# Kernel tuning notes

Hardware: AMD Instinct MI355X
Metric: run time of the kernel (lower is better)

Reference implementation:

```python
import jax, jax.numpy as jnp
import numpy as np
from jax import lax

THRESHOLDS = (0.25, 0.5, 0.75)
TAU = 100.0
NUM_CLASSES = 10
K = 32
RES_Z = 5.0
# each of the 16 binary logic gates is bilinear: g(a,b) = c0 + c1*a + c2*b + c3*a*b
GATE_COEF = jnp.array([
    [0, 0, 0, 0],   # 0: False
    [0, 0, 0, 1],   # 1: a AND b
    [0, 1, 0, -1],  # 2: a AND NOT b
    [0, 1, 0, 0],   # 3: a  (residual gate)
    [0, 0, 1, -1],  # 4: NOT a AND b
    [0, 0, 1, 0],   # 5: b
    [0, 1, 1, -2],  # 6: XOR
    [0, 1, 1, -1],  # 7: OR
    [1, -1, -1, 1], # 8: NOR
    [1, -1, -1, 2], # 9: XNOR
    [1, 0, -1, 0],  # 10: NOT b
    [1, 0, -1, 1],  # 11: a OR NOT b
    [1, -1, 0, 0],  # 12: NOT a
    [1, -1, 0, 1],  # 13: NOT a OR b
    [1, 0, 0, -1],  # 14: NAND
    [1, 0, 0, 0],   # 15: True
], dtype=jnp.float32)


def _gate_logits(key, shape):
    # residual init: pass-through gate (id 3) dominates
    w = 0.01 * jax.random.normal(key, shape, dtype=jnp.float32)
    return w.at[..., 3].add(RES_Z)


def _leaf_idx(rng, C, O, leaves=8, cpt=2, kk=9):
    # each tree uses cpt random input channels; each leaf picks one of them and a 3x3 position
    ch2 = rng.integers(0, C, size=(O, cpt))
    sel = rng.integers(0, cpt, size=(O, leaves))
    ch = np.take_along_axis(ch2, sel, axis=1)
    pos = rng.integers(0, kk, size=(O, leaves))
    return jnp.asarray(ch * kk + pos, dtype=jnp.int32)


def setup_inputs() -> dict:
    key = jax.random.key(0)
    ks = jax.random.split(key, 9)
    rng = np.random.default_rng(0)
    B = 128
    d = {"x": jax.random.uniform(ks[0], (B, 3, 32, 32), dtype=jnp.float32)}
    in_chs = [3 * len(THRESHOLDS), K, 4 * K, 16 * K]
    out_chs = [K, 4 * K, 16 * K, 32 * K]
    for i, (ci, co) in enumerate(zip(in_chs, out_chs)):
        d[f"c{i+1}_idx"] = _leaf_idx(rng, ci, co)
        d[f"c{i+1}_w"] = _gate_logits(ks[1 + i], (co, 7, 16))
    dims = [32 * K * 4, 1280 * K, 640 * K, 320 * K]
    for i in range(3):
        di, do = dims[i], dims[i + 1]
        d[f"l{i+1}_a"] = jnp.asarray(rng.integers(0, di, size=(do,)), dtype=jnp.int32)
        d[f"l{i+1}_b"] = jnp.asarray(rng.integers(0, di, size=(do,)), dtype=jnp.int32)
        d[f"l{i+1}_w"] = _gate_logits(ks[5 + i], (do, 16))
    return d


def _mix(logits):
    # softmax over 16 gates folded into 4 bilinear coefficients (fused gate mixture)
    return jax.nn.softmax(logits, axis=-1) @ GATE_COEF


def binarize(x):
    return jnp.concatenate([(x > t).astype(x.dtype) for t in THRESHOLDS], axis=1)


def tree_conv(x, leaf_idx, logits):
    # x: (B,C,H,W); leaf_idx: (O,8) into C*9 channel-major patch; logits: (O,7,16)
    B, C, H, W = x.shape
    xp = jnp.pad(x, ((0, 0), (0, 0), (1, 1), (1, 1)))
    patches = jnp.stack([xp[:, :, i:i + H, j:j + W] for i in range(3) for j in range(3)], axis=2)
    patches = patches.reshape(B, C * 9, H, W)
    vals = patches[:, leaf_idx]  # (B,O,8,H,W)
    m = _mix(logits)             # (O,7,4)
    node = 0
    for lvl in (4, 2, 1):
        a, b = vals[:, :, 0::2], vals[:, :, 1::2]
        w = m[:, node:node + lvl]  # (O,lvl,4)
        w0 = w[..., 0][None, :, :, None, None]
        w1 = w[..., 1][None, :, :, None, None]
        w2 = w[..., 2][None, :, :, None, None]
        w3 = w[..., 3][None, :, :, None, None]
        vals = w0 + w1 * a + w2 * b + w3 * (a * b)
        node += lvl
    return vals[:, :, 0]  # (B,O,H,W)


def or_pool(x):
    # OR of relaxed binary values == max pool 2x2/2
    return lax.reduce_window(x, -jnp.inf, lax.max, (1, 1, 2, 2), (1, 1, 2, 2), "VALID")


def logic_layer(x, a_idx, b_idx, logits):
    a = x[:, a_idx]  # (B,O)
    b = x[:, b_idx]
    w = _mix(logits)  # (O,4)
    return w[:, 0] + w[:, 1] * a + w[:, 2] * b + w[:, 3] * (a * b)


def group_sum(x):
    B = x.shape[0]
    return x.reshape(B, NUM_CLASSES, -1).sum(axis=-1) / TAU


def reference(x, c1_idx, c1_w, c2_idx, c2_w, c3_idx, c3_w, c4_idx, c4_w,
              l1_a, l1_b, l1_w, l2_a, l2_b, l2_w, l3_a, l3_b, l3_w):
    h = binarize(x)
    h = or_pool(tree_conv(h, c1_idx, c1_w))
    h = or_pool(tree_conv(h, c2_idx, c2_w))
    h = or_pool(tree_conv(h, c3_idx, c3_w))
    h = or_pool(tree_conv(h, c4_idx, c4_w))
    h = h.reshape(h.shape[0], -1)  # (B, 4096)
    h = logic_layer(h, l1_a, l1_b, l1_w)
    h = logic_layer(h, l2_a, l2_b, l2_w)
    h = logic_layer(h, l3_a, l3_b, l3_w)
    return group_sum(h)  # (B, 10)
```

## Files before the change

### kernel.cpp

```cpp
#include <hip/hip_runtime.h>

#define BATCH 128

typedef float v2f __attribute__((ext_vector_type(2)));
typedef float v4f __attribute__((ext_vector_type(4)));

__device__ __constant__ float GC[16][4] = {
  {0,0,0,0},{0,0,0,1},{0,1,0,-1},{0,1,0,0},
  {0,0,1,-1},{0,0,1,0},{0,1,1,-2},{0,1,1,-1},
  {1,-1,-1,1},{1,-1,-1,2},{1,0,-1,0},{1,0,-1,1},
  {1,-1,0,0},{1,-1,0,1},{1,0,0,-1},{1,0,0,0}};

__device__ __forceinline__ v2f pk_mul(v2f a, v2f b) {
  v2f d;
  asm("v_pk_mul_f32 %0, %1, %2" : "=v"(d) : "v"(a), "v"(b));
  return d;
}
__device__ __forceinline__ v2f max2(v2f a, v2f b) {
  v2f d;
  d.x = fmaxf(a.x, b.x);
  d.y = fmaxf(a.y, b.y);
  return d;
}
__device__ __forceinline__ v2f gate2pk(v2f a, v2f b, v2f w01, v2f w23) {
  v2f t = pk_mul(a, b);
  v2f d;
  asm("v_pk_fma_f32 %0, %1, %2, %2 op_sel:[0,1,0] op_sel_hi:[1,1,0]"
      : "=v"(d) : "v"(a), "v"(w01));
  asm("v_pk_fma_f32 %0, %1, %2, %0 op_sel:[0,0,0] op_sel_hi:[1,0,1]"
      : "+v"(d) : "v"(b), "v"(w23));
  asm("v_pk_fma_f32 %0, %1, %2, %0 op_sel:[0,1,0] op_sel_hi:[1,1,1]"
      : "+v"(d) : "v"(t), "v"(w23));
  return d;
}

__device__ __forceinline__ void mix_one(const float* lp, float* op) {
  float e[16];
  float s = 0.f;
  #pragma unroll
  for (int i = 0; i < 16; ++i) { e[i] = __expf(lp[i]); s += e[i]; }
  float inv = 1.0f / s;
  float w0 = 0.f, w1 = 0.f, w2 = 0.f, w3 = 0.f;
  #pragma unroll
  for (int i = 0; i < 16; ++i) {
    float p = e[i] * inv;
    w0 = fmaf(p, GC[i][0], w0);
    w1 = fmaf(p, GC[i][1], w1);
    w2 = fmaf(p, GC[i][2], w2);
    w3 = fmaf(p, GC[i][3], w3);
  }
  op[0] = w0; op[1] = w1; op[2] = w2; op[3] = w3;
}

struct PrepArgs {
  const float* x;
  const float* logits[7];
  float* outm[7];
  float* xtb;
};

__global__ __launch_bounds__(256) void prep_k(PrepArgs A) {
  __shared__ float tile[64 * 129];
  int blk = blockIdx.x;
  if (blk < 327) {
    int gid = blk * 256 + threadIdx.x;
    const int n[7] = {224, 896, 3584, 7168, 40960, 20480, 10240};
    if (gid < 83552) {
      int g = gid, seg = 0;
      while (seg < 6 && g >= n[seg]) { g -= n[seg]; ++seg; }
      mix_one(A.logits[seg] + (size_t)g * 16, A.outm[seg] + (size_t)g * 4);
    }
  } else {
    int tb = blk - 327;
    int c    = tb / 16;
    int pix0 = (tb % 16) * 64;
    int ti = c / 3, rgb = c - ti * 3;
    float th = 0.25f * (float)(ti + 1);
    {
      int pix = threadIdx.x & 63;
      int b0  = threadIdx.x >> 6;
      #pragma unroll 4
      for (int i = 0; i < 32; ++i) {
        int b = b0 + i * 4;
        float xv = A.x[(size_t)(b * 3 + rgb) * 1024 + pix0 + pix];
        tile[pix * 129 + b] = (xv > th) ? 1.f : 0.f;
      }
    }
    __syncthreads();
    {
      int b  = threadIdx.x & 127;
      int p0 = threadIdx.x >> 7;
      #pragma unroll 4
      for (int i = 0; i < 32; ++i) {
        int pix = p0 + i * 2;
        A.xtb[(size_t)(c * 1024 + pix0 + pix) * BATCH + b] = tile[pix * 129 + b];
      }
    }
  }
}

template <int H, int W>
__global__ __launch_bounds__(256) void conv_t(
    const float* __restrict__ in_t, const int* __restrict__ li_g,
    const float* __restrict__ m, float* __restrict__ out_t) {
  constexpr int PH = H / 2, PWD = W / 2, PIX = PH * PWD;
  int wave = threadIdx.x >> 6;
  int b2   = threadIdx.x & 63;
  int q = __builtin_amdgcn_readfirstlane(blockIdx.x * 4 + wave);
  int o = q / PIX;
  int p = q - o * PIX;
  int ph = p / PWD;
  int pw = p - ph * PWD;

  const int* li = li_g + o * 8;
  const v4f* mv = (const v4f*)(m + o * 28);
  v4f g0 = mv[0], g1 = mv[1], g2 = mv[2], g3 = mv[3];
  v4f g4 = mv[4], g5 = mv[5], g6 = mv[6];

  v2f best = {-1e30f, -1e30f};
  #pragma unroll
  for (int half = 0; half < 2; ++half) {
    v2f v[2][8];
    #pragma unroll
    for (int l = 0; l < 8; ++l) {
      int idx = li[l];
      int c = idx / 9;
      int k = idx - c * 9;
      int di = k / 3 - 1;
      int dj = (k - (k / 3) * 3) - 1;
      const float* base = in_t + (size_t)(c * H * W) * BATCH;
      int y = 2 * ph + half + di;
      #pragma unroll
      for (int pi = 0; pi < 2; ++pi) {
        int x = 2 * pw + pi + dj;
        v2f val = {0.f, 0.f};
        if ((unsigned)y < (unsigned)H && (unsigned)x < (unsigned)W)
          val = ((const v2f*)(base + (size_t)(y * W + x) * BATCH))[b2];
        v[pi][l] = val;
      }
    }
    #pragma unroll
    for (int pi = 0; pi < 2; ++pi) {
      v2f u0 = gate2pk(v[pi][0], v[pi][1], g0.xy, g0.zw);
      v2f u1 = gate2pk(v[pi][2], v[pi][3], g1.xy, g1.zw);
      v2f u2 = gate2pk(v[pi][4], v[pi][5], g2.xy, g2.zw);
      v2f u3 = gate2pk(v[pi][6], v[pi][7], g3.xy, g3.zw);
      v2f s0 = gate2pk(u0, u1, g4.xy, g4.zw);
      v2f s1 = gate2pk(u2, u3, g5.xy, g5.zw);
      v2f r  = gate2pk(s0, s1, g6.xy, g6.zw);
      best = max2(best, r);
    }
  }
  ((v2f*)(out_t + (size_t)q * BATCH))[b2] = best;
}

struct LFArgs {
  const float* h4;
  const int *l1a, *l1b, *l2a, *l2b, *l3a, *l3b;
  const float *ml1, *ml2, *ml3;
  float* part;
};

__global__ __launch_bounds__(256) void logic_fused_k(LFArgs A) {
  __shared__ v2f red[4][64];
  int wave = threadIdx.x >> 6;
  int b2   = threadIdx.x & 63;
  int base = __builtin_amdgcn_readfirstlane(blockIdx.x * 32 + wave * 8);

  v2f s = {0.f, 0.f};
  #pragma unroll
  for (int it = 0; it < 8; ++it) {
    int j  = base + it;
    int a3 = A.l3a[j];
    int b3 = A.l3b[j];
    int xa = A.l2a[a3], xb = A.l2b[a3];
    int ya = A.l2a[b3], yb = A.l2b[b3];

    v4f wxa = ((const v4f*)A.ml1)[xa];
    v4f wxb = ((const v4f*)A.ml1)[xb];
    v4f wya = ((const v4f*)A.ml1)[ya];
    v4f wyb = ((const v4f*)A.ml1)[yb];
    v4f wa  = ((const v4f*)A.ml2)[a3];
    v4f wb  = ((const v4f*)A.ml2)[b3];
    v4f wj  = ((const v4f*)A.ml3)[j];

    const float* h4 = A.h4;
    v2f hxa0 = ((const v2f*)(h4 + (size_t)A.l1a[xa] * BATCH))[b2];
    v2f hxa1 = ((const v2f*)(h4 + (size_t)A.l1b[xa] * BATCH))[b2];
    v2f hxb0 = ((const v2f*)(h4 + (size_t)A.l1a[xb] * BATCH))[b2];
    v2f hxb1 = ((const v2f*)(h4 + (size_t)A.l1b[xb] * BATCH))[b2];
    v2f hya0 = ((const v2f*)(h4 + (size_t)A.l1a[ya] * BATCH))[b2];
    v2f hya1 = ((const v2f*)(h4 + (size_t)A.l1b[ya] * BATCH))[b2];
    v2f hyb0 = ((const v2f*)(h4 + (size_t)A.l1a[yb] * BATCH))[b2];
    v2f hyb1 = ((const v2f*)(h4 + (size_t)A.l1b[yb] * BATCH))[b2];

    v2f g1xa = gate2pk(hxa0, hxa1, wxa.xy, wxa.zw);
    v2f g1xb = gate2pk(hxb0, hxb1, wxb.xy, wxb.zw);
    v2f g1ya = gate2pk(hya0, hya1, wya.xy, wya.zw);
    v2f g1yb = gate2pk(hyb0, hyb1, wyb.xy, wyb.zw);
    v2f g2a  = gate2pk(g1xa, g1xb, wa.xy, wa.zw);
    v2f g2b  = gate2pk(g1ya, g1yb, wb.xy, wb.zw);
    s += gate2pk(g2a, g2b, wj.xy, wj.zw);
  }
  red[wave][b2] = s;
  __syncthreads();
  if (threadIdx.x < 64) {
    v2f t = red[0][b2] + red[1][b2] + red[2][b2] + red[3][b2];
    ((v2f*)(A.part + (size_t)blockIdx.x * BATCH))[b2] = t;
  }
}

__global__ __launch_bounds__(128) void gsum_final_k(
    const float* __restrict__ part, float* __restrict__ out) {
  int cls = blockIdx.x;
  int b   = threadIdx.x;
  const float* p = part + (size_t)cls * 32 * BATCH + b;
  float s = 0.f;
  #pragma unroll
  for (int k = 0; k < 32; ++k) s += p[(size_t)k * BATCH];
  out[b * 10 + cls] = s * 0.01f;
}

extern "C" void kernel_launch(void* const* d_in, const int* in_sizes, int n_in,
                              void* d_out, int out_size, void* d_ws, size_t ws_size,
                              hipStream_t stream) {
  const float* x   = (const float*)d_in[0];
  const int*   c1i = (const int*)d_in[1];
  const float* c1w = (const float*)d_in[2];
  const int*   c2i = (const int*)d_in[3];
  const float* c2w = (const float*)d_in[4];
  const int*   c3i = (const int*)d_in[5];
  const float* c3w = (const float*)d_in[6];
  const int*   c4i = (const int*)d_in[7];
  const float* c4w = (const float*)d_in[8];
  const int*   l1a = (const int*)d_in[9];
  const int*   l1b = (const int*)d_in[10];
  const float* l1w = (const float*)d_in[11];
  const int*   l2a = (const int*)d_in[12];
  const int*   l2b = (const int*)d_in[13];
  const float* l2w = (const float*)d_in[14];
  const int*   l3a = (const int*)d_in[15];
  const int*   l3b = (const int*)d_in[16];
  const float* l3w = (const float*)d_in[17];

  float* ws = (float*)d_ws;
  float* mc1 = ws;
  float* mc2 = mc1 + 896;
  float* mc3 = mc2 + 3584;
  float* mc4 = mc3 + 14336;
  float* ml1 = mc4 + 28672;
  float* ml2 = ml1 + 163840;
  float* ml3 = ml2 + 81920;
  float* xtb = ml3 + 40960;
  float* h1  = xtb + 1179648;
  float* h2  = h1 + 1048576;
  float* h3  = h2 + 1048576;
  float* h4  = h3 + 1048576;
  float* part = h4 + 524288;

  PrepArgs A;
  A.x = x;
  A.logits[0] = c1w; A.outm[0] = mc1;
  A.logits[1] = c2w; A.outm[1] = mc2;
  A.logits[2] = c3w; A.outm[2] = mc3;
  A.logits[3] = c4w; A.outm[3] = mc4;
  A.logits[4] = l1w; A.outm[4] = ml1;
  A.logits[5] = l2w; A.outm[5] = ml2;
  A.logits[6] = l3w; A.outm[6] = ml3;
  A.xtb = xtb;
  prep_k<<<471, 256, 0, stream>>>(A);

  conv_t<32, 32><<<8192 / 4, 256, 0, stream>>>(xtb, c1i, mc1, h1);
  conv_t<16, 16><<<8192 / 4, 256, 0, stream>>>(h1, c2i, mc2, h2);
  conv_t<8, 8><<<8192 / 4, 256, 0, stream>>>(h2, c3i, mc3, h3);
  conv_t<4, 4><<<4096 / 4, 256, 0, stream>>>(h3, c4i, mc4, h4);

  LFArgs L;
  L.h4 = h4;
  L.l1a = l1a; L.l1b = l1b;
  L.l2a = l2a; L.l2b = l2b;
  L.l3a = l3a; L.l3b = l3b;
  L.ml1 = ml1; L.ml2 = ml2; L.ml3 = ml3;
  L.part = part;
  logic_fused_k<<<320, 256, 0, stream>>>(L);

  gsum_final_k<<<10, 128, 0, stream>>>(part, (float*)d_out);
}
```

Baseline: 161.1 us.

## Store binarized input and conv intermediates in fp16 to halve gather traffic

Changes the transposed binarized input and all conv-layer activation buffers (h1..h4) from fp32 to fp16. Loads are converted back to fp32 for the gate arithmetic, and results are rounded to fp16 on store. This halves the bytes moved by the gather-heavy conv and logic kernels, which are likely memory or latency bound. The cost is reduced precision of the relaxed activations passed between layers, which may move outputs slightly against the reference.

```diff
diff --git a/kernel.cpp b/kernel.cpp
--- a/kernel.cpp
+++ b/kernel.cpp
@@ -4,6 +4,8 @@
 
 typedef float v2f __attribute__((ext_vector_type(2)));
 typedef float v4f __attribute__((ext_vector_type(4)));
+typedef _Float16 f16;
+typedef _Float16 h2 __attribute__((ext_vector_type(2)));
 
 __device__ __constant__ float GC[16][4] = {
   {0,0,0,0},{0,0,0,1},{0,1,0,-1},{0,1,0,0},
@@ -56,7 +58,7 @@
   const float* x;
   const float* logits[7];
   float* outm[7];
-  float* xtb;
+  f16* xtb;
 };
 
 __global__ __launch_bounds__(256) void prep_k(PrepArgs A) {
@@ -88,12 +90,15 @@
     }
     __syncthreads();
     {
-      int b  = threadIdx.x & 127;
-      int p0 = threadIdx.x >> 7;
+      int b2 = threadIdx.x & 63;
+      int p0 = threadIdx.x >> 6;
       #pragma unroll 4
-      for (int i = 0; i < 32; ++i) {
-        int pix = p0 + i * 2;
-        A.xtb[(size_t)(c * 1024 + pix0 + pix) * BATCH + b] = tile[pix * 129 + b];
+      for (int i = 0; i < 16; ++i) {
+        int pix = p0 + i * 4;
+        h2 hv;
+        hv.x = (f16)tile[pix * 129 + 2 * b2];
+        hv.y = (f16)tile[pix * 129 + 2 * b2 + 1];
+        ((h2*)A.xtb)[(size_t)(c * 1024 + pix0 + pix) * 64 + b2] = hv;
       }
     }
   }
@@ -101,8 +106,8 @@
 
 template <int H, int W>
 __global__ __launch_bounds__(256) void conv_t(
-    const float* __restrict__ in_t, const int* __restrict__ li_g,
-    const float* __restrict__ m, float* __restrict__ out_t) {
+    const f16* __restrict__ in_t, const int* __restrict__ li_g,
+    const float* __restrict__ m, f16* __restrict__ out_t) {
   constexpr int PH = H / 2, PWD = W / 2, PIX = PH * PWD;
   int wave = threadIdx.x >> 6;
   int b2   = threadIdx.x & 63;
@@ -128,14 +133,16 @@
       int k = idx - c * 9;
       int di = k / 3 - 1;
       int dj = (k - (k / 3) * 3) - 1;
-      const float* base = in_t + (size_t)(c * H * W) * BATCH;
+      const h2* base = (const h2*)in_t + (size_t)(c * H * W) * 64 + b2;
       int y = 2 * ph + half + di;
       #pragma unroll
       for (int pi = 0; pi < 2; ++pi) {
         int x = 2 * pw + pi + dj;
         v2f val = {0.f, 0.f};
-        if ((unsigned)y < (unsigned)H && (unsigned)x < (unsigned)W)
-          val = ((const v2f*)(base + (size_t)(y * W + x) * BATCH))[b2];
+        if ((unsigned)y < (unsigned)H && (unsigned)x < (unsigned)W) {
+          h2 hv = base[(size_t)(y * W + x) * 64];
+          val = __builtin_convertvector(hv, v2f);
+        }
         v[pi][l] = val;
       }
     }
@@ -151,11 +158,14 @@
       best = max2(best, r);
     }
   }
-  ((v2f*)(out_t + (size_t)q * BATCH))[b2] = best;
+  h2 hb;
+  hb.x = (f16)best.x;
+  hb.y = (f16)best.y;
+  ((h2*)out_t)[(size_t)q * 64 + b2] = hb;
 }
 
 struct LFArgs {
-  const float* h4;
+  const f16* h4;
   const int *l1a, *l1b, *l2a, *l2b, *l3a, *l3b;
   const float *ml1, *ml2, *ml3;
   float* part;
@@ -167,6 +177,7 @@
   int b2   = threadIdx.x & 63;
   int base = __builtin_amdgcn_readfirstlane(blockIdx.x * 32 + wave * 8);
 
+  const h2* h4 = (const h2*)A.h4;
   v2f s = {0.f, 0.f};
   #pragma unroll
   for (int it = 0; it < 8; ++it) {
@@ -184,15 +195,14 @@
     v4f wb  = ((const v4f*)A.ml2)[b3];
     v4f wj  = ((const v4f*)A.ml3)[j];
 
-    const float* h4 = A.h4;
-    v2f hxa0 = ((const v2f*)(h4 + (size_t)A.l1a[xa] * BATCH))[b2];
-    v2f hxa1 = ((const v2f*)(h4 + (size_t)A.l1b[xa] * BATCH))[b2];
-    v2f hxb0 = ((const v2f*)(h4 + (size_t)A.l1a[xb] * BATCH))[b2];
-    v2f hxb1 = ((const v2f*)(h4 + (size_t)A.l1b[xb] * BATCH))[b2];
-    v2f hya0 = ((const v2f*)(h4 + (size_t)A.l1a[ya] * BATCH))[b2];
-    v2f hya1 = ((const v2f*)(h4 + (size_t)A.l1b[ya] * BATCH))[b2];
-    v2f hyb0 = ((const v2f*)(h4 + (size_t)A.l1a[yb] * BATCH))[b2];
-    v2f hyb1 = ((const v2f*)(h4 + (size_t)A.l1b[yb] * BATCH))[b2];
+    v2f hxa0 = __builtin_convertvector(h4[(size_t)A.l1a[xa] * 64 + b2], v2f);
+    v2f hxa1 = __builtin_convertvector(h4[(size_t)A.l1b[xa] * 64 + b2], v2f);
+    v2f hxb0 = __builtin_convertvector(h4[(size_t)A.l1a[xb] * 64 + b2], v2f);
+    v2f hxb1 = __builtin_convertvector(h4[(size_t)A.l1b[xb] * 64 + b2], v2f);
+    v2f hya0 = __builtin_convertvector(h4[(size_t)A.l1a[ya] * 64 + b2], v2f);
+    v2f hya1 = __builtin_convertvector(h4[(size_t)A.l1b[ya] * 64 + b2], v2f);
+    v2f hyb0 = __builtin_convertvector(h4[(size_t)A.l1a[yb] * 64 + b2], v2f);
+    v2f hyb1 = __builtin_convertvector(h4[(size_t)A.l1b[yb] * 64 + b2], v2f);
 
     v2f g1xa = gate2pk(hxa0, hxa1, wxa.xy, wxa.zw);
     v2f g1xb = gate2pk(hxb0, hxb1, wxb.xy, wxb.zw);
@@ -251,12 +261,12 @@
   float* ml1 = mc4 + 28672;
   float* ml2 = ml1 + 163840;
   float* ml3 = ml2 + 81920;
-  float* xtb = ml3 + 40960;
-  float* h1  = xtb + 1179648;
-  float* h2  = h1 + 1048576;
-  float* h3  = h2 + 1048576;
-  float* h4  = h3 + 1048576;
-  float* part = h4 + 524288;
+  f16* xtb = (f16*)(ml3 + 40960);
+  f16* h1  = xtb + 1179648;
+  f16* h2p = h1 + 1048576;
+  f16* h3  = h2p + 1048576;
+  f16* h4  = h3 + 1048576;
+  float* part = (float*)(h4 + 524288);
 
   PrepArgs A;
   A.x = x;
@@ -271,8 +281,8 @@
   prep_k<<<471, 256, 0, stream>>>(A);
 
   conv_t<32, 32><<<8192 / 4, 256, 0, stream>>>(xtb, c1i, mc1, h1);
-  conv_t<16, 16><<<8192 / 4, 256, 0, stream>>>(h1, c2i, mc2, h2);
-  conv_t<8, 8><<<8192 / 4, 256, 0, stream>>>(h2, c3i, mc3, h3);
+  conv_t<16, 16><<<8192 / 4, 256, 0, stream>>>(h1, c2i, mc2, h2p);
+  conv_t<8, 8><<<8192 / 4, 256, 0, stream>>>(h2p, c3i, mc3, h3);
   conv_t<4, 4><<<4096 / 4, 256, 0, stream>>>(h3, c4i, mc4, h4);
 
   LFArgs L;
```

Measured after the change: 179.7 us. +11.5%, slower.
